# Kernel tuning notes

Measured on AMD Instinct MI355X. Metric: run time of the kernel, lower is better.

The kernel has to match this reference:

```python
import jax, jax.numpy as jnp
import numpy as np

B, DIM, H, W = 8, 64, 64, 64
N_EMBED = 512
NNZ = 4          # num_nonzero OMP iterations
REG = 1e-7       # tiny Tikhonov term for the batched normal-equation solves


def batch_omp(X, D, S):
    """Batch OMP: for each signal pick S atoms greedily and solve LS on support.
    X: [N, d] signals, D: [d, K] dictionary with unit-norm atoms.
    Returns dense sparse code [N, K] with <= S nonzeros per row.
    Mathematically equivalent to the incremental-Cholesky Batch_OMP: at each
    step we solve G_II gamma = alpha0_I on the current support I.
    """
    N, K = X.shape[0], D.shape[1]
    G = D.T @ D                 # [K, K] Gram matrix (precomputed once)
    alpha0 = X @ D              # [N, K] initial correlations D^T x
    alpha = alpha0
    idx_cols = []
    gamma = None
    idx = None
    for k in range(S):          # static small loop over sparsity level
        j = jnp.argmax(jnp.abs(alpha), axis=1)                # [N] greedy atom
        idx_cols.append(j)
        idx = jnp.stack(idx_cols, axis=1)                     # [N, k+1]
        G_sub = G[idx[:, :, None], idx[:, None, :]]           # [N, k+1, k+1]
        rhs = jnp.take_along_axis(alpha0, idx, axis=1)        # [N, k+1]
        reg = REG * jnp.eye(k + 1, dtype=G.dtype)
        gamma = jnp.linalg.solve(G_sub + reg, rhs[..., None])[..., 0]  # [N, k+1]
        # residual correlations: alpha = alpha0 - G[:, I] gamma  (G symmetric)
        alpha = alpha0 - jnp.einsum('nak,na->nk', G[idx], gamma)
    code = jnp.zeros((N, K), X.dtype).at[jnp.arange(N)[:, None], idx].set(gamma)
    return code


def setup_inputs() -> dict:
    key = jax.random.key(0)
    kx, kd = jax.random.split(key)
    x = jax.random.normal(kx, (B, DIM, H, W), dtype=jnp.float32)
    dictionary = jax.random.normal(kd, (DIM, N_EMBED), dtype=jnp.float32)
    return {"x": x, "dictionary": dictionary}


def reference(x, dictionary):
    perm = jnp.transpose(x, (0, 2, 3, 1))            # [B, H, W, C]
    flat = perm.reshape(-1, DIM)                     # [N, C], N = B*H*W
    # normalize_dict=True: atoms normalized to unit L2 norm (in-place in torch)
    Dn = dictionary / jnp.linalg.norm(dictionary, axis=0, keepdims=True)
    code = batch_omp(flat, Dn, NNZ)                  # [N, K] (torch keeps [K, N])
    quant = (code @ Dn.T).reshape(perm.shape)        # reconstruction
    diff_enc = jnp.mean((quant - perm) ** 2)
    diff_dict = diff_enc                             # backward_dict=False branch
    # straight-through: perm + (quant - perm).detach() == quant in value
    out = jnp.transpose(quant, (0, 3, 1, 2))         # [B, C, H, W]
    ids = jnp.transpose(code.reshape(B, H, W, N_EMBED), (0, 3, 1, 2))  # [B, K, H, W]
    norm_0 = jnp.sum(code != 0, axis=1).astype(jnp.float32)  # L0 per signal, [N]
    num_steps = jnp.float32(NNZ)
    mean_D = jnp.mean(jnp.abs(Dn))
    mean_Z = jnp.mean(jnp.abs(code))
    norm_Z = jnp.mean(norm_0)
    topk_num = max(1, int(norm_0.shape[0] * 0.01))   # static: 327
    top_percentile = jnp.min(jax.lax.top_k(norm_0, topk_num)[0])
    num_zeros = jnp.sum(norm_0 == 0).astype(jnp.float32)
    return (out, diff_enc, diff_dict, ids, num_steps, mean_D, mean_Z,
            norm_Z, top_percentile, num_zeros)
```

## Files before the change

### kernel.cpp

```cpp
#include <hip/hip_runtime.h>
#include <cstdint>
#include <cstddef>

#define BQ 8
#define CDIM 64
#define HQ 64
#define WQ 64
#define KDIM 512
#define N_SIG 32768
#define S_NNZ 4

#define DIFF_ENC_OFF 2097152
#define DIFF_DICT_OFF 2097153
#define IDS_OFF 2097154
#define NUM_STEPS_OFF 18874370
#define MEAN_D_OFF 18874371
#define MEAN_Z_OFF 18874372
#define NORM_Z_OFF 18874373
#define TOP_PCT_OFF 18874374
#define NUM_ZEROS_OFF 18874375

#define WS_PD 16
#define WS_DNT 24
#define WS_G 32792
#define WS_WG 294936
#define WS_WI 426008

#define DNR_OFF 4194304

typedef float v2f __attribute__((ext_vector_type(2)));

__global__ __launch_bounds__(256) void k_g(const float* __restrict__ D,
                                           float* __restrict__ G,
                                           float* __restrict__ DnT,
                                           float* __restrict__ pd,
                                           float* __restrict__ Dnr,
                                           float* __restrict__ W) {
  __shared__ float Xs[64 * 64];
  __shared__ float Dns[64 * 64];
  __shared__ float partA[4][64];
  __shared__ float partB[4][64];
  __shared__ float invA[64];
  __shared__ float invB[64];
  int tid = threadIdx.x;
  int w = tid & 63, cq = tid >> 6;
  int ty = tid >> 4, tx = tid & 15;
  if (blockIdx.x == 0 && tid < 16) ((unsigned int*)W)[tid] = 0u;

  int ti = (int)blockIdx.x >> 3, tj = (int)blockIdx.x & 7;
#pragma unroll
  for (int p = 0; p < 16; ++p) {
    int c = p * 4 + cq;
    Xs[c * 64 + w] = D[(size_t)c * KDIM + ti * 64 + w];
    Dns[c * 64 + w] = D[(size_t)c * KDIM + tj * 64 + w];
  }
  __syncthreads();
  float ssA = 0.f, ssB = 0.f;
#pragma unroll
  for (int cc = 0; cc < 16; ++cc) {
    int c = cq * 16 + cc;
    float a = Xs[c * 64 + w];
    ssA = fmaf(a, a, ssA);
    float bv = Dns[c * 64 + w];
    ssB = fmaf(bv, bv, ssB);
  }
  partA[cq][w] = ssA;
  partB[cq][w] = ssB;
  __syncthreads();
  if (tid < 64) {
    invA[tid] = 1.0f / sqrtf(partA[0][tid] + partA[1][tid] + partA[2][tid] + partA[3][tid]);
    invB[tid] = 1.0f / sqrtf(partB[0][tid] + partB[1][tid] + partB[2][tid] + partB[3][tid]);
  }
  __syncthreads();
  if (ti == tj) {
    int kl = tid >> 2, cp = (tid & 3) * 16;
    float ia = invA[kl];
    int kg = ti * 64 + kl;
    float sabs = 0.f;
#pragma unroll
    for (int i = 0; i < 16; ++i) {
      int c = cp + i;
      float v = Xs[c * 64 + kl] * ia;
      DnT[(size_t)kg * CDIM + c] = v;
      Dnr[(size_t)c * KDIM + kg] = v;
      sabs += fabsf(v);
    }
#pragma unroll
    for (int off = 32; off >= 1; off >>= 1) sabs += __shfl_xor(sabs, off);
    __syncthreads();
    if ((tid & 63) == 0) partA[0][tid >> 6] = sabs;
    __syncthreads();
    if (tid == 0) pd[ti] = partA[0][0] + partA[0][1] + partA[0][2] + partA[0][3];
  }
  v2f acc[4][2] = {};
  for (int c = 0; c < 64; ++c) {
    float4 avv = *(const float4*)&Xs[c * 64 + ty * 4];
    float av[4] = {avv.x, avv.y, avv.z, avv.w};
    float4 bv = *(const float4*)&Dns[c * 64 + tx * 4];
    v2f b0 = {bv.x, bv.y}, b1 = {bv.z, bv.w};
#pragma unroll
    for (int i = 0; i < 4; ++i) {
      v2f a2 = {av[i], av[i]};
      acc[i][0] = __builtin_elementwise_fma(a2, b0, acc[i][0]);
      acc[i][1] = __builtin_elementwise_fma(a2, b1, acc[i][1]);
    }
  }
  float sn[4] = {invB[tx * 4], invB[tx * 4 + 1], invB[tx * 4 + 2], invB[tx * 4 + 3]};
#pragma unroll
  for (int i = 0; i < 4; ++i) {
    float im = invA[ty * 4 + i];
    float4 st = make_float4(acc[i][0].x * im * sn[0], acc[i][0].y * im * sn[1],
                            acc[i][1].x * im * sn[2], acc[i][1].y * im * sn[3]);
    *(float4*)&G[(size_t)(ti * 64 + ty * 4 + i) * KDIM + tj * 64 + tx * 4] = st;
  }
}

__device__ __forceinline__ float wave_absmax_u(float m) {
#define DPP_MAX(ctrl)                                                              \
  {                                                                                \
    int t_ = __builtin_amdgcn_update_dpp(0, __float_as_int(m), (ctrl), 0xf, 0xf,   \
                                         true);                                    \
    m = fmaxf(m, __int_as_float(t_));                                              \
  }
  DPP_MAX(0x111) DPP_MAX(0x112) DPP_MAX(0x114) DPP_MAX(0x118)
  DPP_MAX(0x142) DPP_MAX(0x143)
#undef DPP_MAX
  return __int_as_float(__builtin_amdgcn_readlane(__float_as_int(m), 63));
}

template <int SZ>
__device__ __forceinline__ void solve_sz(const float (&gs)[4][4], const float (&rhs)[4],
                                         float (&gamma)[4]) {
  float M[SZ][SZ];
  float y[SZ];
  float idg[SZ];
#pragma unroll
  for (int a = 0; a < SZ; ++a) {
    y[a] = rhs[a];
#pragma unroll
    for (int b = 0; b < SZ; ++b) M[a][b] = gs[a][b] + (a == b ? 1e-7f : 0.0f);
  }
#pragma unroll
  for (int p = 0; p < SZ; ++p) {
    float ip = __builtin_amdgcn_rcpf(M[p][p]);
    idg[p] = ip;
#pragma unroll
    for (int r = p + 1; r < SZ; ++r) {
      float f = M[r][p] * ip;
#pragma unroll
      for (int c = p + 1; c < SZ; ++c) M[r][c] = fmaf(-f, M[p][c], M[r][c]);
      y[r] = fmaf(-f, y[p], y[r]);
    }
  }
#pragma unroll
  for (int r = SZ - 1; r >= 0; --r) {
    float t = y[r];
#pragma unroll
    for (int c = r + 1; c < SZ; ++c) t = fmaf(-M[r][c], gamma[c], t);
    gamma[r] = t * idg[r];
  }
}

template <int K>
__device__ __forceinline__ void omp_step3(int lane, const float* __restrict__ G,
                                          const float* as_row,
                                          float (&al)[8], float (&Grow)[3][8],
                                          float (&gs)[4][4], float (&rhs)[4],
                                          int (&idx)[4], float (&gamma)[4]) {
  float mx0 = fabsf(al[0]);
  int mi = 0;
#pragma unroll
  for (int m = 1; m < 8; ++m) {
    float v = fabsf(al[m]);
    mi = (v > mx0) ? m : mi;
    mx0 = fmaxf(v, mx0);
  }
  float mx = wave_absmax_u(mx0);
  unsigned long long bm = __ballot(mx0 == mx);
  int wl = (int)__builtin_ctzll(bm);
  int mwin = __builtin_amdgcn_readlane(mi, wl);
  int sk = wl * 8 + mwin;
  idx[K] = sk;

  const float* grow_base = G + (size_t)sk * KDIM;
  float4 p0, p1;
  if constexpr (K < 3) {
    p0 = *(const float4*)&as_row[lane * 8];
    p1 = *(const float4*)&as_row[lane * 8 + 4];
  }
  if constexpr (K < 3) {
    const float4* gp = (const float4*)(grow_base + lane * 8);
    float4 r0 = gp[0], r1 = gp[1];
    Grow[K][0] = r0.x; Grow[K][1] = r0.y; Grow[K][2] = r0.z; Grow[K][3] = r0.w;
    Grow[K][4] = r1.x; Grow[K][5] = r1.y; Grow[K][6] = r1.z; Grow[K][7] = r1.w;
  }

#pragma unroll
  for (int b2 = 0; b2 < K; ++b2) {
    float v = grow_base[idx[b2]];
    gs[K][b2] = v;
    gs[b2][K] = v;
  }
  gs[K][K] = grow_base[sk];
  rhs[K] = as_row[sk];

  solve_sz<K + 1>(gs, rhs, gamma);

  if constexpr (K < 3) {
    float a0v[8] = {p0.x, p0.y, p0.z, p0.w, p1.x, p1.y, p1.z, p1.w};
#pragma unroll
    for (int m = 0; m < 8; ++m) {
      float acc2 = a0v[m];
#pragma unroll
      for (int a = 0; a <= K; ++a) acc2 = fmaf(-gamma[a], Grow[a][m], acc2);
      al[m] = acc2;
    }
  }
}

__global__ __launch_bounds__(256, 8) void k_fused(const float* __restrict__ X,
                                                  const float* __restrict__ Dnr,
                                                  const float* __restrict__ G,
                                                  float4* __restrict__ wg,
                                                  int4* __restrict__ wi) {
  __shared__ __align__(16) float AS[8 * 512];
  int tid = threadIdx.x;
  int lane = tid & 63;
  int wv = __builtin_amdgcn_readfirstlane(tid >> 6);
  int bid = (int)blockIdx.x;
  int bh = bid >> 3, w0 = (bid & 7) * 8;
  int b = bh >> 6, h = bh & 63;

  v2f acc[8] = {};
  const v2f* dp = (const v2f*)Dnr + wv * 64 + lane;
  const float* xbase = X + ((size_t)b * CDIM * HQ + h) * WQ + w0;
#pragma unroll 4
  for (int c = 0; c < 64; ++c) {
    v2f d = dp[c * 256];
    const float4* xp = (const float4*)(xbase + (size_t)c * (HQ * WQ));
    float4 x0 = xp[0], x1 = xp[1];
    float xv[8] = {x0.x, x0.y, x0.z, x0.w, x1.x, x1.y, x1.z, x1.w};
#pragma unroll
    for (int s = 0; s < 8; ++s) {
      v2f xx = {xv[s], xv[s]};
      acc[s] = __builtin_elementwise_fma(xx, d, acc[s]);
    }
  }

#pragma unroll
  for (int s = 0; s < 8; ++s)
    *(v2f*)&AS[s * 512 + wv * 128 + lane * 2] = acc[s];
  __syncthreads();

#pragma unroll 1
  for (int s = 0; s < 2; ++s) {
    int sb = wv * 2 + s;
    int n = bid * 8 + sb;
    const float* as_row = &AS[sb * 512];
    float4 q0 = *(const float4*)&as_row[lane * 8];
    float4 q1 = *(const float4*)&as_row[lane * 8 + 4];
    float al[8] = {q0.x, q0.y, q0.z, q0.w, q1.x, q1.y, q1.z, q1.w};
    float Grow[3][8];
    float gs[4][4];
    float rhs[4];
    int idx[4];
    float gamma[4];
    omp_step3<0>(lane, G, as_row, al, Grow, gs, rhs, idx, gamma);
    omp_step3<1>(lane, G, as_row, al, Grow, gs, rhs, idx, gamma);
    omp_step3<2>(lane, G, as_row, al, Grow, gs, rhs, idx, gamma);
    omp_step3<3>(lane, G, as_row, al, Grow, gs, rhs, idx, gamma);
    bool k0 = (idx[0] != idx[1]) && (idx[0] != idx[2]) && (idx[0] != idx[3]);
    bool k1 = (idx[1] != idx[2]) && (idx[1] != idx[3]);
    bool k2 = (idx[2] != idx[3]);
    if (lane == 0) {
      wg[n] = make_float4(k0 ? gamma[0] : 0.f, k1 ? gamma[1] : 0.f,
                          k2 ? gamma[2] : 0.f, gamma[3]);
      wi[n] = make_int4(idx[0], idx[1], idx[2], idx[3]);
    }
  }
}

__global__ __launch_bounds__(256) void k_ei(const float* __restrict__ X,
                                            const float* __restrict__ DnT,
                                            const float4* __restrict__ wg,
                                            const int4* __restrict__ wi,
                                            float* __restrict__ out,
                                            double* __restrict__ accs,
                                            int* __restrict__ hist) {
  __shared__ int sIs[4][64];
  __shared__ float sKs[4][64];
  __shared__ float q[64 * 65];
  __shared__ float red[4];
  int tid = threadIdx.x;

  if (blockIdx.x < 512) {
    int bh = blockIdx.x;
    int b = bh >> 6, h = bh & 63;
    if (tid < 64) {
      int w = tid;
      int n = bh * 64 + w;
      int4 iv = wi[n];
      float4 gv = wg[n];
      sIs[0][w] = iv.x; sIs[1][w] = iv.y; sIs[2][w] = iv.z; sIs[3][w] = iv.w;
      sKs[0][w] = gv.x; sKs[1][w] = gv.y; sKs[2][w] = gv.z; sKs[3][w] = gv.w;
      int nz = (int)(gv.x != 0.f) + (int)(gv.y != 0.f) +
               (int)(gv.z != 0.f) + (int)(gv.w != 0.f);
      float s = fabsf(gv.x) + fabsf(gv.y) + fabsf(gv.z) + fabsf(gv.w);
#pragma unroll
      for (int off = 32; off >= 1; off >>= 1) s += __shfl_xor(s, off);
#pragma unroll
      for (int v = 0; v < 5; ++v) {
        unsigned long long m = __ballot(nz == v);
        if (tid == 0) {
          int c = (int)__popcll(m);
          if (c) atomicAdd(&hist[v], c);
        }
      }
      if (tid == 0) atomicAdd(&accs[0], (double)s);
    }
    __syncthreads();

    int w2 = tid & 63, p = tid >> 6, c0 = p * 16;
    float acc[16] = {};
#pragma unroll
    for (int s = 0; s < 4; ++s) {
      int ks = sIs[s][w2];
      float g = sKs[s][w2];
      const float4* dp = (const float4*)(DnT + (size_t)ks * CDIM + c0);
#pragma unroll
      for (int i4 = 0; i4 < 4; ++i4) {
        float4 d = dp[i4];
        acc[i4 * 4 + 0] = fmaf(g, d.x, acc[i4 * 4 + 0]);
        acc[i4 * 4 + 1] = fmaf(g, d.y, acc[i4 * 4 + 1]);
        acc[i4 * 4 + 2] = fmaf(g, d.z, acc[i4 * 4 + 2]);
        acc[i4 * 4 + 3] = fmaf(g, d.w, acc[i4 * 4 + 3]);
      }
    }
#pragma unroll
    for (int i = 0; i < 16; ++i) q[(c0 + i) * 65 + w2] = acc[i];
    __syncthreads();

    float sumsq = 0.f;
#pragma unroll
    for (int pass = 0; pass < 16; ++pass) {
      int c = pass * 4 + p;
      float qv = q[c * 65 + w2];
      size_t off = (((size_t)b * CDIM + c) * HQ + h) * WQ + w2;
      float xv = X[off];
      float d = qv - xv;
      sumsq = fmaf(d, d, sumsq);
      out[off] = qv;
    }

#pragma unroll
    for (int off = 32; off >= 1; off >>= 1) sumsq += __shfl_xor(sumsq, off);
    if ((tid & 63) == 0) red[tid >> 6] = sumsq;
    __syncthreads();
    if (tid == 0) atomicAdd(&accs[1], (double)(red[0] + red[1] + red[2] + red[3]));
  } else {
    int bid2 = (int)blockIdx.x - 512;
    int b = bid2 >> 8;
    int k0 = (bid2 & 255) * 2;
    float* ids = out + IDS_OFF;
    size_t pbase = ((size_t)b * KDIM + k0) * (HQ * WQ);
#pragma unroll
    for (int r = 0; r < 4; ++r) {
      int pos = r * 1024 + tid * 4;
      int h = pos >> 6;
      int n0 = (b * 64 + h) * 64 + (pos & 63);
      int4 I0 = wi[n0], I1 = wi[n0 + 1], I2 = wi[n0 + 2], I3 = wi[n0 + 3];
      float4 G0 = ((const float4*)wg)[n0];
      float4 G1 = ((const float4*)wg)[n0 + 1];
      float4 G2 = ((const float4*)wg)[n0 + 2];
      float4 G3 = ((const float4*)wg)[n0 + 3];
#pragma unroll
      for (int kk = 0; kk < 2; ++kk) {
        int k = k0 + kk;
        float4 v;
        v.x = (k == I0.w) ? G0.w : (k == I0.z) ? G0.z : (k == I0.y) ? G0.y : (k == I0.x) ? G0.x : 0.f;
        v.y = (k == I1.w) ? G1.w : (k == I1.z) ? G1.z : (k == I1.y) ? G1.y : (k == I1.x) ? G1.x : 0.f;
        v.z = (k == I2.w) ? G2.w : (k == I2.z) ? G2.z : (k == I2.y) ? G2.y : (k == I2.x) ? G2.x : 0.f;
        v.w = (k == I3.w) ? G3.w : (k == I3.z) ? G3.z : (k == I3.y) ? G3.y : (k == I3.x) ? G3.x : 0.f;
        *(float4*)&ids[pbase + (size_t)kk * (HQ * WQ) + pos] = v;
      }
    }
  }
}

__global__ __launch_bounds__(64) void k_final(const double* __restrict__ accs,
                                              const int* __restrict__ hist,
                                              const float* __restrict__ pd,
                                              float* __restrict__ out) {
  if (threadIdx.x == 0) {
    float sumAbsD = 0.f;
#pragma unroll
    for (int i = 0; i < 8; ++i) sumAbsD += pd[i];
    double sumAbsZ = accs[0], sumSq = accs[1];
    float diff = (float)(sumSq / 2097152.0);
    out[DIFF_ENC_OFF] = diff;
    out[DIFF_DICT_OFF] = diff;
    out[NUM_STEPS_OFF] = 4.0f;
    out[MEAN_D_OFF] = sumAbsD / 32768.0f;
    out[MEAN_Z_OFF] = (float)(sumAbsZ / 16777216.0);
    int h0 = hist[0], h1 = hist[1], h2 = hist[2], h3 = hist[3], h4 = hist[4];
    out[NORM_Z_OFF] = (float)((double)(h1 + 2 * h2 + 3 * h3 + 4 * h4) / 32768.0);
    int cum = 0, res = 0;
    for (int v = 4; v >= 0; --v) {
      cum += hist[v];
      if (cum >= 327) { res = v; break; }
    }
    out[TOP_PCT_OFF] = (float)res;
    out[NUM_ZEROS_OFF] = (float)h0;
  }
}

extern "C" void kernel_launch(void* const* d_in, const int* in_sizes, int n_in,
                              void* d_out, int out_size, void* d_ws, size_t ws_size,
                              hipStream_t stream) {
  (void)in_sizes; (void)n_in; (void)out_size; (void)ws_size;
  const float* X = (const float*)d_in[0];
  const float* D = (const float*)d_in[1];
  float* out = (float*)d_out;
  float* W = (float*)d_ws;
  double* accs = (double*)d_ws;
  int* hist = (int*)W + 4;
  float* pd = W + WS_PD;
  float* DnT = W + WS_DNT;
  float* G = W + WS_G;
  float4* wgam = (float4*)(W + WS_WG);
  int4* widx = (int4*)(W + WS_WI);
  float* Dnr = out + DNR_OFF;

  hipLaunchKernelGGL(k_g, dim3(64), dim3(256), 0, stream, D, G, DnT, pd, Dnr, W);
  hipLaunchKernelGGL(k_fused, dim3(4096), dim3(256), 0, stream, X, Dnr, G, wgam, widx);
  hipLaunchKernelGGL(k_ei, dim3(2560), dim3(256), 0, stream, X, DnT, wgam, widx, out,
                     accs, hist);
  hipLaunchKernelGGL(k_final, dim3(1), dim3(64), 0, stream, accs, hist, pd, out);
}
```

Baseline: 184.2 us.

## Zero ids inside fused OMP kernel and scatter nonzeros instead of dense fill

The dense ids tensor (B*K*H*W floats) is now zero-filled by the k_fused blocks, so those stores overlap with the OMP compute. The k_ei kernel then only scatters the up to four nonzero coefficients per signal, which shrinks its grid from 2560 to 640 blocks. The normalized dictionary buffer moves from the output region into the workspace so the zero-fill does not overwrite it. The scattered stores are uncoalesced, and correctness relies on the zero-fill finishing before the scatter, which holds because the two kernels run in order on the same stream.

```diff
diff --git a/kernel.cpp b/kernel.cpp
--- a/kernel.cpp
+++ b/kernel.cpp
@@ -25,8 +25,7 @@
 #define WS_G 32792
 #define WS_WG 294936
 #define WS_WI 426008
-
-#define DNR_OFF 4194304
+#define WS_DNR 589824
 
 typedef float v2f __attribute__((ext_vector_type(2)));
 
@@ -222,12 +221,22 @@
                                                   const float* __restrict__ Dnr,
                                                   const float* __restrict__ G,
                                                   float4* __restrict__ wg,
-                                                  int4* __restrict__ wi) {
+                                                  int4* __restrict__ wi,
+                                                  float* __restrict__ ids) {
   __shared__ __align__(16) float AS[8 * 512];
   int tid = threadIdx.x;
   int lane = tid & 63;
   int wv = __builtin_amdgcn_readfirstlane(tid >> 6);
   int bid = (int)blockIdx.x;
+
+  {
+    size_t gt4 = ((size_t)bid * 256 + tid) * 4;
+    float4 z = make_float4(0.f, 0.f, 0.f, 0.f);
+#pragma unroll
+    for (int j = 0; j < 4; ++j)
+      *(float4*)&ids[(size_t)j * 4194304 + gt4] = z;
+  }
+
   int bh = bid >> 3, w0 = (bid & 7) * 8;
   int b = bh >> 6, h = bh & 63;
 
@@ -358,32 +367,16 @@
     __syncthreads();
     if (tid == 0) atomicAdd(&accs[1], (double)(red[0] + red[1] + red[2] + red[3]));
   } else {
-    int bid2 = (int)blockIdx.x - 512;
-    int b = bid2 >> 8;
-    int k0 = (bid2 & 255) * 2;
+    int n = ((int)blockIdx.x - 512) * 256 + tid;
+    int4 iv = wi[n];
+    float4 gv = wg[n];
+    int b = n >> 12, hw = n & 4095;
     float* ids = out + IDS_OFF;
-    size_t pbase = ((size_t)b * KDIM + k0) * (HQ * WQ);
-#pragma unroll
-    for (int r = 0; r < 4; ++r) {
-      int pos = r * 1024 + tid * 4;
-      int h = pos >> 6;
-      int n0 = (b * 64 + h) * 64 + (pos & 63);
-      int4 I0 = wi[n0], I1 = wi[n0 + 1], I2 = wi[n0 + 2], I3 = wi[n0 + 3];
-      float4 G0 = ((const float4*)wg)[n0];
-      float4 G1 = ((const float4*)wg)[n0 + 1];
-      float4 G2 = ((const float4*)wg)[n0 + 2];
-      float4 G3 = ((const float4*)wg)[n0 + 3];
-#pragma unroll
-      for (int kk = 0; kk < 2; ++kk) {
-        int k = k0 + kk;
-        float4 v;
-        v.x = (k == I0.w) ? G0.w : (k == I0.z) ? G0.z : (k == I0.y) ? G0.y : (k == I0.x) ? G0.x : 0.f;
-        v.y = (k == I1.w) ? G1.w : (k == I1.z) ? G1.z : (k == I1.y) ? G1.y : (k == I1.x) ? G1.x : 0.f;
-        v.z = (k == I2.w) ? G2.w : (k == I2.z) ? G2.z : (k == I2.y) ? G2.y : (k == I2.x) ? G2.x : 0.f;
-        v.w = (k == I3.w) ? G3.w : (k == I3.z) ? G3.z : (k == I3.y) ? G3.y : (k == I3.x) ? G3.x : 0.f;
-        *(float4*)&ids[pbase + (size_t)kk * (HQ * WQ) + pos] = v;
-      }
-    }
+    size_t pbase = (size_t)b * (KDIM * HQ * WQ) + hw;
+    if (gv.x != 0.f) ids[pbase + (size_t)iv.x * (HQ * WQ)] = gv.x;
+    if (gv.y != 0.f) ids[pbase + (size_t)iv.y * (HQ * WQ)] = gv.y;
+    if (gv.z != 0.f) ids[pbase + (size_t)iv.z * (HQ * WQ)] = gv.z;
+    if (gv.w != 0.f) ids[pbase + (size_t)iv.w * (HQ * WQ)] = gv.w;
   }
 }
 
@@ -429,11 +422,12 @@
   float* G = W + WS_G;
   float4* wgam = (float4*)(W + WS_WG);
   int4* widx = (int4*)(W + WS_WI);
-  float* Dnr = out + DNR_OFF;
+  float* Dnr = W + WS_DNR;
+  float* ids = out + IDS_OFF;
 
   hipLaunchKernelGGL(k_g, dim3(64), dim3(256), 0, stream, D, G, DnT, pd, Dnr, W);
-  hipLaunchKernelGGL(k_fused, dim3(4096), dim3(256), 0, stream, X, Dnr, G, wgam, widx);
-  hipLaunchKernelGGL(k_ei, dim3(2560), dim3(256), 0, stream, X, DnT, wgam, widx, out,
+  hipLaunchKernelGGL(k_fused, dim3(4096), dim3(256), 0, stream, X, Dnr, G, wgam, widx, ids);
+  hipLaunchKernelGGL(k_ei, dim3(640), dim3(256), 0, stream, X, DnT, wgam, widx, out,
                      accs, hist);
   hipLaunchKernelGGL(k_final, dim3(1), dim3(64), 0, stream, accs, hist, pd, out);
 }
```

Result: faster. 175.1 us (-4.9%).
